# Kernel tuning notes

Measured on AMD Instinct MI355X. Metric: run time of the kernel, lower is better.

## Reference

```python
import jax, jax.numpy as jnp
import numpy as np

NUM_HEADS = 8
WIN = (7, 7)


def _relative_position_index(wh, ww):
    # Same construction as the torch module (numpy, static).
    coords = np.stack(np.meshgrid(np.arange(wh), np.arange(ww), indexing='ij'))  # (2, wh, ww)
    flat = coords.reshape(2, -1)                                                 # (2, L)
    rel = flat[:, :, None] - flat[:, None, :]                                    # (2, L, L)
    rel = rel.transpose(1, 2, 0).astype(np.int64)                                # (L, L, 2)
    rel[:, :, 0] += wh - 1
    rel[:, :, 1] += ww - 1
    rel[:, :, 0] *= 2 * ww - 1
    return rel.sum(-1)  # (L, L), values in [0, (2wh-1)*(2ww-1))


def setup_inputs() -> dict:
    key = jax.random.key(0)
    k0, k1, k2, k3, k4 = jax.random.split(key, 5)
    B, C = 2048, 256
    wh, ww = WIN
    L = wh * ww
    nW = 64
    q = jax.random.normal(k0, (B, C, wh, ww), dtype=jnp.float32)
    k = jax.random.normal(k1, (B, C, wh, ww), dtype=jnp.float32)
    v = jax.random.normal(k2, (B, C, wh, ww), dtype=jnp.float32)
    # Swin-style shift mask: 0 where attend, -100 where blocked
    keep = jax.random.uniform(k3, (nW, L, L)) < 0.9
    mask = jnp.where(keep, 0.0, -100.0).astype(jnp.float32)
    n_bias = (2 * wh - 1) * (2 * ww - 1)  # 169
    rel_bias_table = 0.02 * jax.random.normal(k4, (n_bias, NUM_HEADS), dtype=jnp.float32)
    rel_pos_index = jnp.asarray(_relative_position_index(wh, ww), dtype=jnp.int32)
    return {"q": q, "k": k, "v": v, "mask": mask,
            "rel_bias_table": rel_bias_table, "rel_pos_index": rel_pos_index}


def reference(q, k, v, mask, rel_bias_table, rel_pos_index):
    b, c, wh, ww = q.shape
    L = wh * ww
    H = NUM_HEADS
    d_k = c // H
    scale = d_k ** -0.5
    qh = q.reshape(b, H, d_k, L)
    kh = k.reshape(b, H, d_k, L)
    # NOTE: the original torch code reassigns v = k.reshape(...) — values come from k.
    vh = kh
    attn = jnp.einsum('bhct,bhcs->bhts', qh, kh) * scale  # (b, H, L, L)
    bias = rel_bias_table[rel_pos_index.reshape(-1)].reshape(L, L, H)
    attn = attn + jnp.transpose(bias, (2, 0, 1))[None]    # (1, H, L, L)
    nW = mask.shape[0]
    attn = attn.reshape(b // nW, nW, H, L, L) + mask[None, :, None]
    attn = attn.reshape(b, H, L, L)
    attn = jax.nn.softmax(attn, axis=-1)
    score = jnp.einsum('bhts,bhcs->bhct', attn, vh).reshape(b, c, wh, ww)
    return (score, attn)
```

## Files before the change

### kernel.cpp

```cpp
#include <hip/hip_runtime.h>
#include <math.h>


#define LW 49
#define NH 8

typedef short s16x8 __attribute__((ext_vector_type(8)));
typedef float f32x4 __attribute__((ext_vector_type(4)));

union Frag { s16x8 v; unsigned short u[8]; };

__device__ __forceinline__ unsigned short f2bf(float x) {
    unsigned u = __float_as_uint(x);
    u += 0x7FFFu + ((u >> 16) & 1u);
    return (unsigned short)(u >> 16);
}
__device__ __forceinline__ float bf2f(unsigned short h) {
    return __uint_as_float(((unsigned)h) << 16);
}
__device__ __forceinline__ void split8(const float* xf, Frag& hi, Frag& lo) {
    #pragma unroll
    for (int j = 0; j < 8; j++) {
        unsigned short hb = f2bf(xf[j]);
        hi.u[j] = hb;
        lo.u[j] = f2bf(xf[j] - bf2f(hb));
    }
}

#define MFMA16(A, B, C) __builtin_amdgcn_mfma_f32_16x16x32_bf16((A), (B), (C), 0, 0, 0)

__global__ __launch_bounds__(256) void prep_frag_kernel(
    const float* __restrict__ mask, const float* __restrict__ table,
    const int* __restrict__ idx,
    float* __restrict__ biasF, float* __restrict__ maskF)
{
    const int i = blockIdx.x * 256 + threadIdx.x;
    const int NBF = 8 * 4096;
    const int NMF = 64 * 4096;
    if (i < NBF) {
        const int h = i >> 12, rem = i & 4095;
        const int gi = rem >> 8, lane = (rem >> 2) & 63, r = rem & 3;
        const int mt = gi >> 2, nt = gi & 3;
        const int t = mt * 16 + (lane >> 4) * 4 + r;
        const int s = nt * 16 + (lane & 15);
        biasF[i] = (t < LW && s < LW) ? table[idx[t * LW + s] * NH + h] : 0.f;
    } else if (i < NBF + NMF) {
        const int j = i - NBF;
        const int w2 = j >> 12, rem = j & 4095;
        const int gi = rem >> 8, lane = (rem >> 2) & 63, r = rem & 3;
        const int mt = gi >> 2, nt = gi & 3;
        const int t = mt * 16 + (lane >> 4) * 4 + r;
        const int s = nt * 16 + (lane & 15);
        maskF[j] = (t < LW && s < LW) ? mask[w2 * (LW * LW) + t * LW + s] : 0.f;
    }
}

__global__ __launch_bounds__(64, 3) void wa_mfma_kernel(
    const float* __restrict__ q, const float* __restrict__ k,
    const float* __restrict__ biasF, const float* __restrict__ maskF,
    float* __restrict__ score_out, float* __restrict__ attn_out)
{
    __shared__ unsigned sP[64 * 64];

    const int bh   = blockIdx.x;
    const int b    = bh >> 3;
    const int h    = bh & 7;
    const int w    = b & 63;
    const int lane = threadIdx.x;
    const int l15  = lane & 15;
    const int g4   = lane >> 4;

    const float* qp = q + (size_t)bh * (32 * LW);
    const float* kp = k + (size_t)bh * (32 * LW);

    Frag Qh[4], Ql[4];
    #pragma unroll
    for (int mt = 0; mt < 4; mt++) {
        const int t  = mt * 16 + l15;
        const int tc = t < LW ? t : (LW - 1);
        float xf[8];
        #pragma unroll
        for (int j = 0; j < 8; j++) xf[j] = qp[(g4 * 8 + j) * LW + tc];
        split8(xf, Qh[mt], Ql[mt]);
    }

    f32x4 acc[4][4];
    #pragma unroll
    for (int mt = 0; mt < 4; mt++)
        #pragma unroll
        for (int nt = 0; nt < 4; nt++)
            #pragma unroll
            for (int r = 0; r < 4; r++) acc[mt][nt][r] = 0.f;

    #pragma unroll
    for (int nt = 0; nt < 4; nt++) {
        const int s  = nt * 16 + l15;
        const int sc = s < LW ? s : (LW - 1);
        float xf[8];
        #pragma unroll
        for (int j = 0; j < 8; j++) xf[j] = kp[(g4 * 8 + j) * LW + sc];
        Frag Kh, Kl;
        split8(xf, Kh, Kl);
        #pragma unroll
        for (int mt = 0; mt < 4; mt++) {
            acc[mt][nt] = MFMA16(Qh[mt].v, Kh.v, acc[mt][nt]);
            acc[mt][nt] = MFMA16(Ql[mt].v, Kh.v, acc[mt][nt]);
            acc[mt][nt] = MFMA16(Qh[mt].v, Kl.v, acc[mt][nt]);
        }
    }

    const float scale = 0.17677669529663687f;
    const float* bF = biasF + (size_t)h * 4096 + lane * 4;
    const float* mF = maskF + (size_t)w * 4096 + lane * 4;
    #pragma unroll
    for (int mt = 0; mt < 4; mt++) {
        #pragma unroll
        for (int nt = 0; nt < 4; nt++) {
            const int gi = mt * 4 + nt;
            const f32x4 bq = *(const f32x4*)(bF + gi * 256);
            const f32x4 mq = *(const f32x4*)(mF + gi * 256);
            const bool pad = (nt * 16 + l15) >= LW;
            #pragma unroll
            for (int r = 0; r < 4; r++) {
                const float v2 = fmaf(acc[mt][nt][r], scale, bq[r] + mq[r]);
                acc[mt][nt][r] = pad ? -1e30f : v2;
            }
        }
    }

    float inv[4][4];
    #pragma unroll
    for (int mt = 0; mt < 4; mt++) {
        #pragma unroll
        for (int r = 0; r < 4; r++) {
            float mx = fmaxf(fmaxf(acc[mt][0][r], acc[mt][1][r]),
                             fmaxf(acc[mt][2][r], acc[mt][3][r]));
            mx = fmaxf(mx, __shfl_xor(mx, 1));
            mx = fmaxf(mx, __shfl_xor(mx, 2));
            mx = fmaxf(mx, __shfl_xor(mx, 4));
            mx = fmaxf(mx, __shfl_xor(mx, 8));
            float sm = 0.f;
            #pragma unroll
            for (int nt = 0; nt < 4; nt++) {
                const float p = __expf(acc[mt][nt][r] - mx);
                acc[mt][nt][r] = p;
                sm += p;
            }
            sm += __shfl_xor(sm, 1);
            sm += __shfl_xor(sm, 2);
            sm += __shfl_xor(sm, 4);
            sm += __shfl_xor(sm, 8);
            inv[mt][r] = 1.0f / sm;
        }
    }

    float* attn_base = attn_out + (size_t)bh * (LW * LW);
    #pragma unroll
    for (int mt = 0; mt < 4; mt++) {
        #pragma unroll
        for (int r = 0; r < 4; r++) {
            const int t = mt * 16 + g4 * 4 + r;
            const unsigned swz = (((unsigned)t >> 2) & 3u) << 4;
            #pragma unroll
            for (int nt = 0; nt < 4; nt++) {
                const int s = nt * 16 + l15;
                const float p = acc[mt][nt][r] * inv[mt][r];
                const unsigned short ph = f2bf(p);
                const unsigned short pl = f2bf(p - bf2f(ph));
                sP[t * 64 + (s ^ swz)] = (unsigned)ph | ((unsigned)pl << 16);
                if (t < LW && s < LW) attn_base[t * LW + s] = p;
            }
        }
    }

    Frag K2h[2][2], K2l[2][2];
    #pragma unroll
    for (int mt = 0; mt < 2; mt++) {
        const int c = mt * 16 + l15;
        #pragma unroll
        for (int ks = 0; ks < 2; ks++) {
            float xf[8];
            #pragma unroll
            for (int j = 0; j < 8; j++) {
                const int s  = ks * 32 + g4 * 8 + j;
                const int sc = s < LW ? s : (LW - 1);
                xf[j] = kp[c * LW + sc];
            }
            split8(xf, K2h[mt][ks], K2l[mt][ks]);
        }
    }

    f32x4 acc2[2][4];
    #pragma unroll
    for (int mt = 0; mt < 2; mt++)
        #pragma unroll
        for (int nt = 0; nt < 4; nt++)
            #pragma unroll
            for (int r = 0; r < 4; r++) acc2[mt][nt][r] = 0.f;

    #pragma unroll
    for (int nt = 0; nt < 4; nt++) {
        const int t = nt * 16 + l15;
        const unsigned swz = (((unsigned)t >> 2) & 3u) << 4;
        #pragma unroll
        for (int ks = 0; ks < 2; ks++) {
            const int sb = ks * 32 + g4 * 8;
            const uint4* pp = (const uint4*)&sP[t * 64 + (sb ^ swz)];
            const uint4 a0 = pp[0], a1 = pp[1];
            const unsigned pk[8] = {a0.x, a0.y, a0.z, a0.w,
                                    a1.x, a1.y, a1.z, a1.w};
            Frag Ph, Pl;
            #pragma unroll
            for (int e = 0; e < 8; e++) {
                Ph.u[e] = (unsigned short)(pk[e] & 0xFFFFu);
                Pl.u[e] = (unsigned short)(pk[e] >> 16);
            }
            #pragma unroll
            for (int mt = 0; mt < 2; mt++) {
                acc2[mt][nt] = MFMA16(K2h[mt][ks].v, Ph.v, acc2[mt][nt]);
                acc2[mt][nt] = MFMA16(K2l[mt][ks].v, Ph.v, acc2[mt][nt]);
                acc2[mt][nt] = MFMA16(K2h[mt][ks].v, Pl.v, acc2[mt][nt]);
            }
        }
    }

    float* sc = score_out + (size_t)bh * (32 * LW);
    #pragma unroll
    for (int mt = 0; mt < 2; mt++) {
        #pragma unroll
        for (int nt = 0; nt < 4; nt++) {
            const int t = nt * 16 + l15;
            if (t < LW) {
                #pragma unroll
                for (int r = 0; r < 4; r++) {
                    const int c = mt * 16 + g4 * 4 + r;
                    sc[c * LW + t] = acc2[mt][nt][r];
                }
            }
        }
    }
}

__global__ __launch_bounds__(256, 4) void wa_fallback_kernel(
    const float* __restrict__ q, const float* __restrict__ k,
    const float* __restrict__ mask0, const float* __restrict__ table,
    const int* __restrict__ idx,
    float* __restrict__ score_out, float* __restrict__ attn_out)
{
    __shared__ float sPf[LW * LW];
    const int lane = threadIdx.x & 63;
    const int wv   = __builtin_amdgcn_readfirstlane(threadIdx.x >> 6);
    const int bh   = blockIdx.x * 4 + wv;
    const int h    = bh & 7;
    const int w    = (bh >> 3) & 63;
    const int t    = lane;
    const int tc   = (t < LW) ? t : (LW - 1);

    const float* qp = q + (size_t)bh * (32 * LW);
    const float* kp = k + (size_t)bh * (32 * LW);

    float qreg[32];
    #pragma unroll
    for (int c = 0; c < 32; c++) qreg[c] = qp[c * LW + tc];

    float S[LW];
    #pragma unroll
    for (int s = 0; s < LW; s++) S[s] = 0.f;
    #pragma unroll
    for (int c = 0; c < 32; c++) {
        #pragma unroll
        for (int s = 0; s < LW; s++)
            S[s] = fmaf(qreg[c], kp[c * LW + s], S[s]);
    }

    const float scale = 0.17677669529663687f;
    const float* mrow = mask0 + (size_t)w * (LW * LW) + tc * LW;
    const int*   irow = idx + tc * LW;
    #pragma unroll
    for (int s = 0; s < LW; s++) {
        const float bm = table[irow[s] * NH + h] + mrow[s];
        S[s] = fmaf(S[s], scale, bm);
    }

    float m = S[0];
    #pragma unroll
    for (int s = 1; s < LW; s++) m = fmaxf(m, S[s]);
    float sum = 0.f;
    #pragma unroll
    for (int s = 0; s < LW; s++) { S[s] = __expf(S[s] - m); sum += S[s]; }
    const float invs = 1.0f / sum;
    #pragma unroll
    for (int s = 0; s < LW; s++) S[s] *= invs;

    float* attn_base = attn_out + (size_t)bh * (LW * LW);
    for (int turn = 0; turn < 4; turn++) {
        __syncthreads();
        if (turn == wv) {
            if (t < LW) {
                #pragma unroll
                for (int s = 0; s < LW; s++) sPf[t * LW + s] = S[s];
            }
            #pragma unroll
            for (int it = 0; it < 38; it++) {
                const int i = it * 64 + lane;
                if (i < LW * LW) attn_base[i] = sPf[i];
            }
        }
    }

    float* sc = score_out + (size_t)bh * (32 * LW);
    #pragma unroll
    for (int c = 0; c < 32; c++) {
        float a = 0.f;
        #pragma unroll
        for (int s = 0; s < LW; s++) a = fmaf(S[s], kp[c * LW + s], a);
        if (t < LW) sc[c * LW + t] = a;
    }
}

extern "C" void kernel_launch(void* const* d_in, const int* in_sizes, int n_in,
                              void* d_out, int out_size, void* d_ws, size_t ws_size,
                              hipStream_t stream) {
    const float* q     = (const float*)d_in[0];
    const float* k     = (const float*)d_in[1];
    const float* mask  = (const float*)d_in[3];
    const float* table = (const float*)d_in[4];
    const int*   idx   = (const int*)d_in[5];

    float* score_out = (float*)d_out;
    float* attn_out  = score_out + (size_t)2048 * 256 * 49;

    const size_t NBF = (size_t)8 * 4096;
    const size_t NMF = (size_t)64 * 4096;

    if (ws_size >= (NBF + NMF) * sizeof(float)) {
        float* biasF = (float*)d_ws;
        float* maskF = biasF + NBF;
        const int tot = (int)(NBF + NMF);
        prep_frag_kernel<<<(tot + 255) / 256, 256, 0, stream>>>(
            mask, table, idx, biasF, maskF);
        wa_mfma_kernel<<<16384, 64, 0, stream>>>(
            q, k, biasF, maskF, score_out, attn_out);
    } else {
        wa_fallback_kernel<<<4096, 256, 0, stream>>>(
            q, k, mask, table, idx, score_out, attn_out);
    }
}
```

Baseline: 508.1 us.

## Pack two heads per block, truncate bf16 split, stage P in halves, nontemporal stores

Each block now runs two wavefronts, one head each, and the shared P buffer is halved by staging P in two 32-column chunks with a new XOR swizzle. The bf16 hi/lo split now truncates instead of rounding, which takes ALU ops out of the conversion. The K^T fragment loads move ahead of the softmax so they overlap with it. Output stores for attn and score become nontemporal. Truncation makes the split slightly less precise, though the hi+lo residual still keeps most of the accuracy.

```diff
diff --git a/kernel.cpp b/kernel.cpp
--- a/kernel.cpp
+++ b/kernel.cpp
@@ -10,20 +10,13 @@
 
 union Frag { s16x8 v; unsigned short u[8]; };
 
-__device__ __forceinline__ unsigned short f2bf(float x) {
-    unsigned u = __float_as_uint(x);
-    u += 0x7FFFu + ((u >> 16) & 1u);
-    return (unsigned short)(u >> 16);
-}
-__device__ __forceinline__ float bf2f(unsigned short h) {
-    return __uint_as_float(((unsigned)h) << 16);
-}
-__device__ __forceinline__ void split8(const float* xf, Frag& hi, Frag& lo) {
+__device__ __forceinline__ void split8t(const float* xf, Frag& hi, Frag& lo) {
     #pragma unroll
     for (int j = 0; j < 8; j++) {
-        unsigned short hb = f2bf(xf[j]);
-        hi.u[j] = hb;
-        lo.u[j] = f2bf(xf[j] - bf2f(hb));
+        const unsigned u = __float_as_uint(xf[j]);
+        hi.u[j] = (unsigned short)(u >> 16);
+        const float r = xf[j] - __uint_as_float(u & 0xFFFF0000u);
+        lo.u[j] = (unsigned short)(__float_as_uint(r) >> 16);
     }
 }
 
@@ -55,20 +48,21 @@
     }
 }
 
-__global__ __launch_bounds__(64, 3) void wa_mfma_kernel(
+__global__ __launch_bounds__(128, 4) void wa_mfma_kernel(
     const float* __restrict__ q, const float* __restrict__ k,
     const float* __restrict__ biasF, const float* __restrict__ maskF,
     float* __restrict__ score_out, float* __restrict__ attn_out)
 {
-    __shared__ unsigned sP[64 * 64];
-
-    const int bh   = blockIdx.x;
-    const int b    = bh >> 3;
+    __shared__ unsigned sP[2][64 * 32];
+
+    const int wv   = __builtin_amdgcn_readfirstlane((int)(threadIdx.x >> 6));
+    const int bh   = blockIdx.x * 2 + wv;
     const int h    = bh & 7;
-    const int w    = b & 63;
-    const int lane = threadIdx.x;
+    const int w    = (bh >> 3) & 63;
+    const int lane = threadIdx.x & 63;
     const int l15  = lane & 15;
     const int g4   = lane >> 4;
+    unsigned* sPw  = sP[wv];
 
     const float* qp = q + (size_t)bh * (32 * LW);
     const float* kp = k + (size_t)bh * (32 * LW);
@@ -81,7 +75,7 @@
         float xf[8];
         #pragma unroll
         for (int j = 0; j < 8; j++) xf[j] = qp[(g4 * 8 + j) * LW + tc];
-        split8(xf, Qh[mt], Ql[mt]);
+        split8t(xf, Qh[mt], Ql[mt]);
     }
 
     f32x4 acc[4][4];
@@ -100,12 +94,29 @@
         #pragma unroll
         for (int j = 0; j < 8; j++) xf[j] = kp[(g4 * 8 + j) * LW + sc];
         Frag Kh, Kl;
-        split8(xf, Kh, Kl);
+        split8t(xf, Kh, Kl);
         #pragma unroll
         for (int mt = 0; mt < 4; mt++) {
             acc[mt][nt] = MFMA16(Qh[mt].v, Kh.v, acc[mt][nt]);
             acc[mt][nt] = MFMA16(Ql[mt].v, Kh.v, acc[mt][nt]);
             acc[mt][nt] = MFMA16(Qh[mt].v, Kl.v, acc[mt][nt]);
+        }
+    }
+
+    Frag K2h[2][2], K2l[2][2];
+    #pragma unroll
+    for (int mt = 0; mt < 2; mt++) {
+        const int c = mt * 16 + l15;
+        #pragma unroll
+        for (int ks = 0; ks < 2; ks++) {
+            float xf[8];
+            #pragma unroll
+            for (int j = 0; j < 8; j++) {
+                const int s  = ks * 32 + g4 * 8 + j;
+                const int sc = s < LW ? s : (LW - 1);
+                xf[j] = kp[c * LW + sc];
+            }
+            split8t(xf, K2h[mt][ks], K2l[mt][ks]);
         }
     }
 
@@ -160,33 +171,14 @@
         #pragma unroll
         for (int r = 0; r < 4; r++) {
             const int t = mt * 16 + g4 * 4 + r;
-            const unsigned swz = (((unsigned)t >> 2) & 3u) << 4;
             #pragma unroll
             for (int nt = 0; nt < 4; nt++) {
                 const int s = nt * 16 + l15;
                 const float p = acc[mt][nt][r] * inv[mt][r];
-                const unsigned short ph = f2bf(p);
-                const unsigned short pl = f2bf(p - bf2f(ph));
-                sP[t * 64 + (s ^ swz)] = (unsigned)ph | ((unsigned)pl << 16);
-                if (t < LW && s < LW) attn_base[t * LW + s] = p;
-            }
-        }
-    }
-
-    Frag K2h[2][2], K2l[2][2];
-    #pragma unroll
-    for (int mt = 0; mt < 2; mt++) {
-        const int c = mt * 16 + l15;
-        #pragma unroll
-        for (int ks = 0; ks < 2; ks++) {
-            float xf[8];
-            #pragma unroll
-            for (int j = 0; j < 8; j++) {
-                const int s  = ks * 32 + g4 * 8 + j;
-                const int sc = s < LW ? s : (LW - 1);
-                xf[j] = kp[c * LW + sc];
-            }
-            split8(xf, K2h[mt][ks], K2l[mt][ks]);
+                acc[mt][nt][r] = p;
+                if (t < LW && s < LW)
+                    __builtin_nontemporal_store(p, &attn_base[t * LW + s]);
+            }
         }
     }
 
@@ -199,14 +191,32 @@
             for (int r = 0; r < 4; r++) acc2[mt][nt][r] = 0.f;
 
     #pragma unroll
-    for (int nt = 0; nt < 4; nt++) {
-        const int t = nt * 16 + l15;
-        const unsigned swz = (((unsigned)t >> 2) & 3u) << 4;
-        #pragma unroll
-        for (int ks = 0; ks < 2; ks++) {
-            const int sb = ks * 32 + g4 * 8;
-            const uint4* pp = (const uint4*)&sP[t * 64 + (sb ^ swz)];
-            const uint4 a0 = pp[0], a1 = pp[1];
+    for (int ks = 0; ks < 2; ks++) {
+        #pragma unroll
+        for (int mt = 0; mt < 4; mt++) {
+            #pragma unroll
+            for (int r = 0; r < 4; r++) {
+                const int t = mt * 16 + g4 * 4 + r;
+                const unsigned sw = ((unsigned)t & 7u) << 2;
+                #pragma unroll
+                for (int ntl = 0; ntl < 2; ntl++) {
+                    const float p  = acc[mt][2 * ks + ntl][r];
+                    const unsigned pu = __float_as_uint(p);
+                    const float rl = p - __uint_as_float(pu & 0xFFFF0000u);
+                    const unsigned w32 = (pu >> 16) |
+                                         (__float_as_uint(rl) & 0xFFFF0000u);
+                    const unsigned sl = (unsigned)(ntl * 16 + l15);
+                    sPw[(unsigned)t * 32u + (sl ^ sw)] = w32;
+                }
+            }
+        }
+        #pragma unroll
+        for (int ntt = 0; ntt < 4; ntt++) {
+            const int t = ntt * 16 + l15;
+            const unsigned sw = ((unsigned)t & 7u) << 2;
+            const unsigned baseA = (unsigned)t * 32u + (((unsigned)g4 * 8u) ^ sw);
+            const uint4 a0 = *(const uint4*)&sPw[baseA];
+            const uint4 a1 = *(const uint4*)&sPw[baseA ^ 4u];
             const unsigned pk[8] = {a0.x, a0.y, a0.z, a0.w,
                                     a1.x, a1.y, a1.z, a1.w};
             Frag Ph, Pl;
@@ -217,9 +227,9 @@
             }
             #pragma unroll
             for (int mt = 0; mt < 2; mt++) {
-                acc2[mt][nt] = MFMA16(K2h[mt][ks].v, Ph.v, acc2[mt][nt]);
-                acc2[mt][nt] = MFMA16(K2l[mt][ks].v, Ph.v, acc2[mt][nt]);
-                acc2[mt][nt] = MFMA16(K2h[mt][ks].v, Pl.v, acc2[mt][nt]);
+                acc2[mt][ntt] = MFMA16(K2h[mt][ks].v, Ph.v, acc2[mt][ntt]);
+                acc2[mt][ntt] = MFMA16(K2l[mt][ks].v, Ph.v, acc2[mt][ntt]);
+                acc2[mt][ntt] = MFMA16(K2h[mt][ks].v, Pl.v, acc2[mt][ntt]);
             }
         }
     }
@@ -234,7 +244,8 @@
                 #pragma unroll
                 for (int r = 0; r < 4; r++) {
                     const int c = mt * 16 + g4 * 4 + r;
-                    sc[c * LW + t] = acc2[mt][nt][r];
+                    __builtin_nontemporal_store(acc2[mt][nt][r],
+                                                &sc[c * LW + t]);
                 }
             }
         }
@@ -249,7 +260,7 @@
 {
     __shared__ float sPf[LW * LW];
     const int lane = threadIdx.x & 63;
-    const int wv   = __builtin_amdgcn_readfirstlane(threadIdx.x >> 6);
+    const int wv   = __builtin_amdgcn_readfirstlane((int)(threadIdx.x >> 6));
     const int bh   = blockIdx.x * 4 + wv;
     const int h    = bh & 7;
     const int w    = (bh >> 3) & 63;
@@ -339,7 +350,7 @@
         const int tot = (int)(NBF + NMF);
         prep_frag_kernel<<<(tot + 255) / 256, 256, 0, stream>>>(
             mask, table, idx, biasF, maskF);
-        wa_mfma_kernel<<<16384, 64, 0, stream>>>(
+        wa_mfma_kernel<<<8192, 128, 0, stream>>>(
             q, k, biasF, maskF, score_out, attn_out);
     } else {
         wa_fallback_kernel<<<4096, 256, 0, stream>>>(
```

New measurement: 584.9 us. +15.1%, slower.
